# Kernel tuning notes

Measured on AMD Instinct MI355X. Metric: run time of the kernel, lower is better.

Reference implementation:

```python
import jax, jax.numpy as jnp
import numpy as np

N, F, H, D, E, G = 100000, 128, 2, 32, 1600000, 2048
HD = H * D
NEG_SLOPE = 0.2


def setup_inputs() -> dict:
    key = jax.random.key(0)
    ks = jax.random.split(key, 9)
    node = jax.random.normal(ks[0], (N, F), jnp.float32)
    edge_index = jax.random.randint(ks[1], (2, E), 0, N, dtype=jnp.int32)
    batch = jnp.sort(jax.random.randint(ks[2], (N,), 0, G, dtype=jnp.int32))
    # GATConv params
    W_gat = jax.random.normal(ks[3], (F, HD), jnp.float32) * (1.0 / np.sqrt(F))
    att_src = jax.random.normal(ks[4], (H, D), jnp.float32) * (1.0 / np.sqrt(D))
    att_dst = jax.random.normal(ks[5], (H, D), jnp.float32) * (1.0 / np.sqrt(D))
    bias_gat = jnp.zeros((HD,), jnp.float32)
    # SAGPooling score GNN = GraphConv(HD -> 1)
    W_rel = jax.random.normal(ks[6], (HD, 1), jnp.float32) * (1.0 / np.sqrt(HD))
    b_rel = jnp.zeros((1,), jnp.float32)
    W_root = jax.random.normal(ks[7], (HD, 1), jnp.float32) * (1.0 / np.sqrt(HD))
    return dict(node=node, edge_index=edge_index, batch=batch, W_gat=W_gat,
                att_src=att_src, att_dst=att_dst, bias_gat=bias_gat,
                W_rel=W_rel, b_rel=b_rel, W_root=W_root)


def _segment_softmax(logits, seg, num_segments):
    m = jax.ops.segment_max(logits, seg, num_segments=num_segments)
    e = jnp.exp(logits - m[seg])
    s = jax.ops.segment_sum(e, seg, num_segments=num_segments)
    return e / s[seg]


def reference(node, edge_index, batch, W_gat, att_src, att_dst, bias_gat,
              W_rel, b_rel, W_root):
    # ---- GATConv (heads=H, concat) with self-loops (PyG default) ----
    loops = jnp.arange(N, dtype=edge_index.dtype)
    src = jnp.concatenate([edge_index[0], loops])   # [E+N]
    dst = jnp.concatenate([edge_index[1], loops])   # [E+N]
    xw = (node @ W_gat).reshape(N, H, D)            # [N,H,D]
    a_src = jnp.einsum('nhd,hd->nh', xw, att_src)   # [N,H]
    a_dst = jnp.einsum('nhd,hd->nh', xw, att_dst)   # [N,H]
    logits = jax.nn.leaky_relu(a_src[src] + a_dst[dst], NEG_SLOPE)  # [E+N,H]
    alpha = _segment_softmax(logits, dst, N)        # softmax over incoming edges
    msg = xw[src] * alpha[:, :, None]               # [E+N,H,D]
    x = jax.ops.segment_sum(msg, dst, num_segments=N).reshape(N, HD) + bias_gat

    # ---- SAGPooling(min_score=-1): GraphConv score, per-graph softmax ----
    # GraphConv: out_i = W_root x_i + W_rel * sum_{j->i} x_j + b
    agg = jax.ops.segment_sum(x[edge_index[0]], edge_index[1], num_segments=N)
    score = (agg @ W_rel + b_rel + x @ W_root).reshape(-1)  # [N]
    score = _segment_softmax(score, batch, G)
    # min_score=-1 and softmax(score) >= 0 => all nodes survive top-k filter
    att_x = x * score[:, None]

    # ---- global_add_pool ----
    global_graph_emb = jax.ops.segment_sum(att_x, batch, num_segments=G)  # [G,HD]
    return (x, global_graph_emb)
```

## Files before the change

### kernel.cpp

```cpp
#include <hip/hip_runtime.h>
#include <hip/hip_fp16.h>

#define N_NODES 100000
#define F_IN    128
#define HDIM    64
#define NE      1600000
#define NG      2048
#define NEG_SLOPE 0.2f
#define DCAP    48
#define NB      3125
#define BCAP    768
#define NS2     512
#define SE2     (NE / NS2)
#define SCB     64
#define SCT     128

typedef unsigned short ushort_t;
typedef short bf16x8 __attribute__((ext_vector_type(8)));
typedef float f32x4 __attribute__((ext_vector_type(4)));

__device__ __forceinline__ ushort_t f2bf(float x) {
    unsigned u = __float_as_uint(x);
    unsigned r = u + 0x7fffu + ((u >> 16) & 1u);
    return (ushort_t)(r >> 16);
}
__device__ __forceinline__ float bf2f(ushort_t b) {
    return __uint_as_float(((unsigned)b) << 16);
}
__device__ __forceinline__ float f16lo(unsigned u) {
    __half hh = *(__half*)&u;
    return __half2float(hh);
}


__global__ __launch_bounds__(256) void k_hist(const int* __restrict__ ei,
        int* __restrict__ hist, const float* __restrict__ Wg,
        ushort_t* __restrict__ Wpack, const int* __restrict__ batch,
        int* __restrict__ gstart) {
    __shared__ int hc[NB];
    int t = threadIdx.x, b = blockIdx.x;
    if (b < NS2) {
        for (int i = t; i < NB; i += 256) hc[i] = 0;
        __syncthreads();
        int e0 = b * SE2;
        for (int e = e0 + t; e < e0 + SE2; e += 256)
            atomicAdd(&hc[ei[NE + e] >> 5], 1);
        __syncthreads();
        for (int i = t; i < NB; i += 256) hist[b * NB + i] = hc[i];
    } else if (b < NS2 + 32) {
        int i = (b - NS2) * 256 + t;
        int frag = i >> 9, lane = (i >> 3) & 63, j = i & 7;
        int ct = frag >> 2, kt = frag & 3;
        int k = kt * 32 + (lane >> 4) * 8 + j;
        int c = ct * 16 + (lane & 15);
        Wpack[i] = f2bf(Wg[k * HDIM + c]);
    } else {
        int n = (b - NS2 - 32) * 256 + t;
        if (n < N_NODES) {
            int bn = batch[n];
            int bp = (n == 0) ? -1 : batch[n - 1];
            for (int g = bp + 1; g <= bn; ++g) gstart[g] = n;
            if (n == N_NODES - 1)
                for (int g = bn + 1; g <= NG; ++g) gstart[g] = N_NODES;
        }
    }
}

__global__ __launch_bounds__(256) void k_scan(int* __restrict__ hist,
        int* __restrict__ bcnt) {
    __shared__ int tile[SCT][SCB + 1];
    int t = threadIdx.x;
    int b0 = blockIdx.x * SCB;
    int col = t & 63;
    int gb = b0 + col;
    bool own = (t < 64) && (gb < NB);
    int carry = own ? gb * BCAP : 0;

    for (int tile0 = 0; tile0 < NS2; tile0 += SCT) {
        for (int r = 0; r < SCT; r += 4) {
            int s = r + (t >> 6);
            int bb = b0 + col;
            tile[s][col] = (bb < NB) ? hist[(tile0 + s) * NB + bb] : 0;
        }
        __syncthreads();
        if (t < 64) {
            int c = carry;
#pragma unroll 8
            for (int s = 0; s < SCT; ++s) {
                int v = tile[s][col];
                tile[s][col] = c;
                c += v;
            }
            carry = c;
        }
        __syncthreads();
        for (int r = 0; r < SCT; r += 4) {
            int s = r + (t >> 6);
            int bb = b0 + col;
            if (bb < NB) hist[(tile0 + s) * NB + bb] = tile[s][col];
        }
        __syncthreads();
    }
    if (own) bcnt[gb] = carry - gb * BCAP;
}

__global__ __launch_bounds__(256) void k_scatter(const int* __restrict__ ei,
        const int* __restrict__ off, int* __restrict__ ebuf) {
    __shared__ int cursor[NB];
    int t = threadIdx.x;
    int bid = blockIdx.x;
    int b = ((bid & 7) << 6) | (bid >> 3);
    for (int i = t; i < NB; i += 256) cursor[i] = off[b * NB + i];
    __syncthreads();
    int e0 = b * SE2;
    for (int e = e0 + t; e < e0 + SE2; e += 256) {
        int d = ei[NE + e];
        int s = ei[e];
        int bb = d >> 5;
        int pos = atomicAdd(&cursor[bb], 1);
        if (pos < (bb + 1) * BCAP) ebuf[pos] = s | ((d & 31) << 17);
    }
}

__global__ __launch_bounds__(256) void k_gemm(const float* __restrict__ node,
        const ushort_t* __restrict__ Wpack, const float* __restrict__ att_s,
        const float* __restrict__ att_d, ushort_t* __restrict__ xw,
        float* __restrict__ a_src, float* __restrict__ a_dst) {
    int t = threadIdx.x;
    int lane = t & 63, w = t >> 6;
    int r0 = blockIdx.x * 64 + w * 16;

    int arow = r0 + (lane & 15);
    int arow_c = arow < N_NODES ? arow : N_NODES - 1;
    const float* nr = node + (size_t)arow_c * F_IN + (lane >> 4) * 8;

    bf16x8 a[4];
#pragma unroll
    for (int kt = 0; kt < 4; ++kt) {
        float4 v0 = *(const float4*)(nr + kt * 32);
        float4 v1 = *(const float4*)(nr + kt * 32 + 4);
        bf16x8 av;
        av[0] = (short)f2bf(v0.x); av[1] = (short)f2bf(v0.y);
        av[2] = (short)f2bf(v0.z); av[3] = (short)f2bf(v0.w);
        av[4] = (short)f2bf(v1.x); av[5] = (short)f2bf(v1.y);
        av[6] = (short)f2bf(v1.z); av[7] = (short)f2bf(v1.w);
        a[kt] = av;
    }

    const bf16x8* wp = (const bf16x8*)Wpack;
    float sv[2][4], dv[2][4];
#pragma unroll
    for (int h = 0; h < 2; ++h)
#pragma unroll
        for (int jj = 0; jj < 4; ++jj) { sv[h][jj] = 0.f; dv[h][jj] = 0.f; }

#pragma unroll
    for (int ct = 0; ct < 4; ++ct) {
        f32x4 acc = {0.f, 0.f, 0.f, 0.f};
#pragma unroll
        for (int kt = 0; kt < 4; ++kt) {
            bf16x8 bfr = wp[(ct * 4 + kt) * 64 + lane];
            acc = __builtin_amdgcn_mfma_f32_16x16x32_bf16(a[kt], bfr, acc, 0, 0, 0);
        }
        int col = ct * 16 + (lane & 15);
        float as_c = att_s[col];
        float ad_c = att_d[col];
        int h = ct >> 1;
#pragma unroll
        for (int jj = 0; jj < 4; ++jj) {
            int r = r0 + (lane >> 4) * 4 + jj;
            if (r < N_NODES) xw[(size_t)r * HDIM + col] = f2bf(acc[jj]);
            sv[h][jj] += acc[jj] * as_c;
            dv[h][jj] += acc[jj] * ad_c;
        }
    }

#pragma unroll
    for (int m = 1; m <= 8; m <<= 1) {
#pragma unroll
        for (int h = 0; h < 2; ++h)
#pragma unroll
            for (int jj = 0; jj < 4; ++jj) {
                sv[h][jj] += __shfl_xor(sv[h][jj], m, 64);
                dv[h][jj] += __shfl_xor(dv[h][jj], m, 64);
            }
    }
    if ((lane & 15) == 0) {
        int g = lane >> 4;
#pragma unroll
        for (int jj = 0; jj < 4; ++jj) {
            int r = r0 + g * 4 + jj;
            if (r < N_NODES) {
                a_src[r * 2 + 0] = sv[0][jj];
                a_src[r * 2 + 1] = sv[1][jj];
                a_dst[r * 2 + 0] = dv[0][jj];
                a_dst[r * 2 + 1] = dv[1][jj];
            }
        }
    }
}

__global__ __launch_bounds__(256) void k_gat(const int* __restrict__ bcnt,
        const int* __restrict__ ebuf, const ushort_t* __restrict__ xw,
        const float* __restrict__ a_src, const float* __restrict__ a_dst,
        const float* __restrict__ bias, const float* __restrict__ wrel,
        const float* __restrict__ wroot, const float* __restrict__ brel,
        float* __restrict__ x_out, float* __restrict__ p,
        float* __restrict__ base) {
    __shared__ int2 rows[32][DCAP];
    __shared__ int rowcnt[32];
    __shared__ float adld[64];
    int t = threadIdx.x, b = blockIdx.x;
    if (t < 32) rowcnt[t] = 0;
    if (t < 64) adld[t] = a_dst[b * 64 + t];
    __syncthreads();

    int cnt = bcnt[b]; if (cnt > BCAP) cnt = BCAP;
    const int* eb = ebuf + b * BCAP;
    for (int i = t; i < cnt; i += 256) {
        int v = eb[i];
        int s = v & 0x1FFFF;
        int dl = v >> 17;
        float2 asp = *(const float2*)(a_src + 2 * s);
        float l0 = asp.x + adld[2 * dl];     l0 = l0 > 0.f ? l0 : NEG_SLOPE * l0;
        float l1 = asp.y + adld[2 * dl + 1]; l1 = l1 > 0.f ? l1 : NEG_SLOPE * l1;
        __half2 hp = __floats2half2_rn(__expf(l0), __expf(l1));
        int pos = atomicAdd(&rowcnt[dl], 1);
        if (pos < DCAP) rows[dl][pos] = make_int2(s, *(int*)&hp);
    }
    __syncthreads();

    int lane = t & 63, wv = t >> 6;
    int h = lane >> 5;
    unsigned shift = (lane & 32) >> 1;
    const ushort_t* xwl = xw + lane;
    float bias_l = bias[lane];
    float wrel_l = wrel[lane];
    float wroot_l = wroot[lane];
    float br = brel[0];

#pragma unroll
    for (int q8 = 0; q8 < 8; ++q8) {
        int dl = wv * 8 + q8;
        int d = b * 32 + dl;
        int nv = rowcnt[dl]; if (nv > DCAP) nv = DCAP;
        const int2* rw = rows[dl];
        float acc = 0.f, den = 0.f;
        int j = 0;
        for (; j + 4 <= nv; j += 4) {
            int2 q0 = rw[j], q1 = rw[j + 1], q2 = rw[j + 2], q3 = rw[j + 3];
            ushort_t x0 = xwl[(size_t)q0.x * HDIM];
            ushort_t x1 = xwl[(size_t)q1.x * HDIM];
            ushort_t x2 = xwl[(size_t)q2.x * HDIM];
            ushort_t x3 = xwl[(size_t)q3.x * HDIM];
            float w0 = f16lo(((unsigned)q0.y) >> shift);
            float w1 = f16lo(((unsigned)q1.y) >> shift);
            float w2 = f16lo(((unsigned)q2.y) >> shift);
            float w3 = f16lo(((unsigned)q3.y) >> shift);
            acc += w0 * bf2f(x0); den += w0;
            acc += w1 * bf2f(x1); den += w1;
            acc += w2 * bf2f(x2); den += w2;
            acc += w3 * bf2f(x3); den += w3;
        }
        for (; j < nv; ++j) {
            int2 q0 = rw[j];
            float w0 = f16lo(((unsigned)q0.y) >> shift);
            acc += w0 * bf2f(xwl[(size_t)q0.x * HDIM]); den += w0;
        }

        float2 asd = *(const float2*)(a_src + 2 * d);
        float lgs = (h ? asd.y : asd.x) + adld[2 * dl + h];
        lgs = lgs > 0.f ? lgs : NEG_SLOPE * lgs;
        float es = __expf(lgs);
        float xself = bf2f(xw[(size_t)d * HDIM + lane]);
        float v = (acc + es * xself) / (den + es) + bias_l;
        x_out[(size_t)d * HDIM + lane] = v;

        float pv = v * wrel_l;
        float rv = v * wroot_l;
#pragma unroll
        for (int m = 32; m >= 1; m >>= 1) {
            pv += __shfl_xor(pv, m, 64);
            rv += __shfl_xor(rv, m, 64);
        }
        if (lane == 0) { p[d] = pv; base[d] = rv + br; }
    }
}

__global__ __launch_bounds__(256) void k_score(const int* __restrict__ bcnt,
        const int* __restrict__ ebuf, const float* __restrict__ pp,
        const float* __restrict__ base, float* __restrict__ evec) {
    __shared__ float sa[32];
    int t = threadIdx.x, b = blockIdx.x;
    if (t < 32) sa[t] = 0.f;
    __syncthreads();
    int cnt = bcnt[b]; if (cnt > BCAP) cnt = BCAP;
    const int* eb = ebuf + b * BCAP;
    for (int i = t; i < cnt; i += 256) {
        int v = eb[i];
        atomicAdd(&sa[v >> 17], pp[v & 0x1FFFF]);
    }
    __syncthreads();
    if (t < 32) {
        int n = b * 32 + t;
        evec[n] = __expf(sa[t] + base[n]);
    }
}

__global__ __launch_bounds__(256) void k_pool(const float* __restrict__ x,
        const float* __restrict__ evec, const int* __restrict__ gstart,
        float* __restrict__ emb) {
    int g = blockIdx.x;
    int lane = threadIdx.x & 63;
    int wave = threadIdx.x >> 6;
    int beg = gstart[g], end = gstart[g + 1];
    float acc = 0.f, esum = 0.f;
    for (int n = beg + wave; n < end; n += 4) {
        float ev = evec[n];
        acc += ev * x[(size_t)n * HDIM + lane];
        esum += ev;
    }
    __shared__ float sacc[4][HDIM];
    __shared__ float ses[4];
    sacc[wave][lane] = acc;
    if (lane == 0) ses[wave] = esum;
    __syncthreads();
    if (wave == 0) {
        float a = sacc[0][lane] + sacc[1][lane] + sacc[2][lane] + sacc[3][lane];
        float es = ses[0] + ses[1] + ses[2] + ses[3];
        emb[(size_t)g * HDIM + lane] = (es > 0.f) ? (a / es) : 0.f;
    }
}

extern "C" void kernel_launch(void* const* d_in, const int* in_sizes, int n_in,
                              void* d_out, int out_size, void* d_ws, size_t ws_size,
                              hipStream_t stream) {
    const float* node  = (const float*)d_in[0];
    const int*   ei    = (const int*)d_in[1];
    const int*   batch = (const int*)d_in[2];
    const float* Wg    = (const float*)d_in[3];
    const float* att_s = (const float*)d_in[4];
    const float* att_d = (const float*)d_in[5];
    const float* bias  = (const float*)d_in[6];
    const float* wrel  = (const float*)d_in[7];
    const float* brel  = (const float*)d_in[8];
    const float* wroot = (const float*)d_in[9];

    float* out = (float*)d_out;
    float* emb = out + (size_t)N_NODES * HDIM;

    float*    ws     = (float*)d_ws;
    ushort_t* Wpack  = (ushort_t*)ws;
    ushort_t* xw     = (ushort_t*)(ws + 4096);
    float*    a_src  = ws + 3204096;
    float*    a_dst  = ws + 3404096;
    float*    p      = ws + 3604096;
    float*    base   = ws + 3704096;
    float*    evec   = ws + 3804096;
    int*      gstart = (int*)(ws + 3904096);
    int*      bcnt   = (int*)(ws + 3906148);
    int*      ebuf   = (int*)(ws + 3909280);
    int*      hist   = (int*)(ws + 6309280);

    k_hist<<<NS2 + 32 + 391, 256, 0, stream>>>(ei, hist, Wg, Wpack, batch, gstart);
    k_scan<<<(NB + SCB - 1) / SCB, 256, 0, stream>>>(hist, bcnt);
    k_scatter<<<NS2, 256, 0, stream>>>(ei, hist, ebuf);
    k_gemm<<<(N_NODES + 63) / 64, 256, 0, stream>>>(node, Wpack, att_s, att_d,
                                                    xw, a_src, a_dst);
    k_gat<<<NB, 256, 0, stream>>>(bcnt, ebuf, xw, a_src, a_dst,
                                  bias, wrel, wroot, brel, out, p, base);
    k_score<<<NB, 256, 0, stream>>>(bcnt, ebuf, p, base, evec);
    k_pool<<<NG, 256, 0, stream>>>(out, evec, gstart, emb);
}
```

Before: 157.9 us.

## Fuse GEMM into front kernel and gather two bf16 columns per lane in GAT

```diff
diff --git a/kernel.cpp b/kernel.cpp
--- a/kernel.cpp
+++ b/kernel.cpp
@@ -14,6 +14,7 @@
 #define SE2     (NE / NS2)
 #define SCB     64
 #define SCT     128
+#define GEMM_BLKS 1563
 
 typedef unsigned short ushort_t;
 typedef short bf16x8 __attribute__((ext_vector_type(8)));
@@ -33,29 +34,107 @@
 }
 
 
-__global__ __launch_bounds__(256) void k_hist(const int* __restrict__ ei,
-        int* __restrict__ hist, const float* __restrict__ Wg,
-        ushort_t* __restrict__ Wpack, const int* __restrict__ batch,
-        int* __restrict__ gstart) {
-    __shared__ int hc[NB];
+__global__ __launch_bounds__(256) void k_front(const float* __restrict__ node,
+        const float* __restrict__ Wg, const float* __restrict__ att_s,
+        const float* __restrict__ att_d, ushort_t* __restrict__ xw,
+        float* __restrict__ a_src, float* __restrict__ a_dst,
+        const int* __restrict__ ei, int* __restrict__ hist,
+        const int* __restrict__ batch, int* __restrict__ gstart) {
+    __shared__ __align__(16) char smem[16384];
     int t = threadIdx.x, b = blockIdx.x;
-    if (b < NS2) {
+    if (b < GEMM_BLKS) {
+        ushort_t* WL = (ushort_t*)smem;
+        for (int i = t; i < 8192; i += 256) {
+            int frag = i >> 9, ln = (i >> 3) & 63, j = i & 7;
+            int ct = frag >> 2, kt = frag & 3;
+            int k = kt * 32 + (ln >> 4) * 8 + j;
+            int c = ct * 16 + (ln & 15);
+            WL[i] = f2bf(Wg[k * HDIM + c]);
+        }
+        __syncthreads();
+
+        int lane = t & 63, w = t >> 6;
+        int r0 = b * 64 + w * 16;
+        int arow = r0 + (lane & 15);
+        int arow_c = arow < N_NODES ? arow : N_NODES - 1;
+        const float* nr = node + (size_t)arow_c * F_IN + (lane >> 4) * 8;
+
+        bf16x8 a[4];
+#pragma unroll
+        for (int kt = 0; kt < 4; ++kt) {
+            float4 v0 = *(const float4*)(nr + kt * 32);
+            float4 v1 = *(const float4*)(nr + kt * 32 + 4);
+            bf16x8 av;
+            av[0] = (short)f2bf(v0.x); av[1] = (short)f2bf(v0.y);
+            av[2] = (short)f2bf(v0.z); av[3] = (short)f2bf(v0.w);
+            av[4] = (short)f2bf(v1.x); av[5] = (short)f2bf(v1.y);
+            av[6] = (short)f2bf(v1.z); av[7] = (short)f2bf(v1.w);
+            a[kt] = av;
+        }
+
+        const bf16x8* wp = (const bf16x8*)WL;
+        float sv[2][4], dv[2][4];
+#pragma unroll
+        for (int h = 0; h < 2; ++h)
+#pragma unroll
+            for (int jj = 0; jj < 4; ++jj) { sv[h][jj] = 0.f; dv[h][jj] = 0.f; }
+
+#pragma unroll
+        for (int ct = 0; ct < 4; ++ct) {
+            f32x4 acc = {0.f, 0.f, 0.f, 0.f};
+#pragma unroll
+            for (int kt = 0; kt < 4; ++kt) {
+                bf16x8 bfr = wp[(ct * 4 + kt) * 64 + lane];
+                acc = __builtin_amdgcn_mfma_f32_16x16x32_bf16(a[kt], bfr, acc, 0, 0, 0);
+            }
+            int col = ct * 16 + (lane & 15);
+            float as_c = att_s[col];
+            float ad_c = att_d[col];
+            int h = ct >> 1;
+#pragma unroll
+            for (int jj = 0; jj < 4; ++jj) {
+                int r = r0 + (lane >> 4) * 4 + jj;
+                if (r < N_NODES) xw[(size_t)r * HDIM + col] = f2bf(acc[jj]);
+                sv[h][jj] += acc[jj] * as_c;
+                dv[h][jj] += acc[jj] * ad_c;
+            }
+        }
+
+#pragma unroll
+        for (int m = 1; m <= 8; m <<= 1) {
+#pragma unroll
+            for (int h = 0; h < 2; ++h)
+#pragma unroll
+                for (int jj = 0; jj < 4; ++jj) {
+                    sv[h][jj] += __shfl_xor(sv[h][jj], m, 64);
+                    dv[h][jj] += __shfl_xor(dv[h][jj], m, 64);
+                }
+        }
+        if ((lane & 15) == 0) {
+            int g = lane >> 4;
+#pragma unroll
+            for (int jj = 0; jj < 4; ++jj) {
+                int r = r0 + g * 4 + jj;
+                if (r < N_NODES) {
+                    a_src[r * 2 + 0] = sv[0][jj];
+                    a_src[r * 2 + 1] = sv[1][jj];
+                    a_dst[r * 2 + 0] = dv[0][jj];
+                    a_dst[r * 2 + 1] = dv[1][jj];
+                }
+            }
+        }
+    } else if (b < GEMM_BLKS + NS2) {
+        int* hc = (int*)smem;
+        int bb = b - GEMM_BLKS;
         for (int i = t; i < NB; i += 256) hc[i] = 0;
         __syncthreads();
-        int e0 = b * SE2;
+        int e0 = bb * SE2;
         for (int e = e0 + t; e < e0 + SE2; e += 256)
             atomicAdd(&hc[ei[NE + e] >> 5], 1);
         __syncthreads();
-        for (int i = t; i < NB; i += 256) hist[b * NB + i] = hc[i];
-    } else if (b < NS2 + 32) {
-        int i = (b - NS2) * 256 + t;
-        int frag = i >> 9, lane = (i >> 3) & 63, j = i & 7;
-        int ct = frag >> 2, kt = frag & 3;
-        int k = kt * 32 + (lane >> 4) * 8 + j;
-        int c = ct * 16 + (lane & 15);
-        Wpack[i] = f2bf(Wg[k * HDIM + c]);
+        for (int i = t; i < NB; i += 256) hist[bb * NB + i] = hc[i];
     } else {
-        int n = (b - NS2 - 32) * 256 + t;
+        int n = (b - GEMM_BLKS - NS2) * 256 + t;
         if (n < N_NODES) {
             int bn = batch[n];
             int bp = (n == 0) ? -1 : batch[n - 1];
@@ -119,84 +198,6 @@
         int bb = d >> 5;
         int pos = atomicAdd(&cursor[bb], 1);
         if (pos < (bb + 1) * BCAP) ebuf[pos] = s | ((d & 31) << 17);
-    }
-}
-
-__global__ __launch_bounds__(256) void k_gemm(const float* __restrict__ node,
-        const ushort_t* __restrict__ Wpack, const float* __restrict__ att_s,
-        const float* __restrict__ att_d, ushort_t* __restrict__ xw,
-        float* __restrict__ a_src, float* __restrict__ a_dst) {
-    int t = threadIdx.x;
-    int lane = t & 63, w = t >> 6;
-    int r0 = blockIdx.x * 64 + w * 16;
-
-    int arow = r0 + (lane & 15);
-    int arow_c = arow < N_NODES ? arow : N_NODES - 1;
-    const float* nr = node + (size_t)arow_c * F_IN + (lane >> 4) * 8;
-
-    bf16x8 a[4];
-#pragma unroll
-    for (int kt = 0; kt < 4; ++kt) {
-        float4 v0 = *(const float4*)(nr + kt * 32);
-        float4 v1 = *(const float4*)(nr + kt * 32 + 4);
-        bf16x8 av;
-        av[0] = (short)f2bf(v0.x); av[1] = (short)f2bf(v0.y);
-        av[2] = (short)f2bf(v0.z); av[3] = (short)f2bf(v0.w);
-        av[4] = (short)f2bf(v1.x); av[5] = (short)f2bf(v1.y);
-        av[6] = (short)f2bf(v1.z); av[7] = (short)f2bf(v1.w);
-        a[kt] = av;
-    }
-
-    const bf16x8* wp = (const bf16x8*)Wpack;
-    float sv[2][4], dv[2][4];
-#pragma unroll
-    for (int h = 0; h < 2; ++h)
-#pragma unroll
-        for (int jj = 0; jj < 4; ++jj) { sv[h][jj] = 0.f; dv[h][jj] = 0.f; }
-
-#pragma unroll
-    for (int ct = 0; ct < 4; ++ct) {
-        f32x4 acc = {0.f, 0.f, 0.f, 0.f};
-#pragma unroll
-        for (int kt = 0; kt < 4; ++kt) {
-            bf16x8 bfr = wp[(ct * 4 + kt) * 64 + lane];
-            acc = __builtin_amdgcn_mfma_f32_16x16x32_bf16(a[kt], bfr, acc, 0, 0, 0);
-        }
-        int col = ct * 16 + (lane & 15);
-        float as_c = att_s[col];
-        float ad_c = att_d[col];
-        int h = ct >> 1;
-#pragma unroll
-        for (int jj = 0; jj < 4; ++jj) {
-            int r = r0 + (lane >> 4) * 4 + jj;
-            if (r < N_NODES) xw[(size_t)r * HDIM + col] = f2bf(acc[jj]);
-            sv[h][jj] += acc[jj] * as_c;
-            dv[h][jj] += acc[jj] * ad_c;
-        }
-    }
-
-#pragma unroll
-    for (int m = 1; m <= 8; m <<= 1) {
-#pragma unroll
-        for (int h = 0; h < 2; ++h)
-#pragma unroll
-            for (int jj = 0; jj < 4; ++jj) {
-                sv[h][jj] += __shfl_xor(sv[h][jj], m, 64);
-                dv[h][jj] += __shfl_xor(dv[h][jj], m, 64);
-            }
-    }
-    if ((lane & 15) == 0) {
-        int g = lane >> 4;
-#pragma unroll
-        for (int jj = 0; jj < 4; ++jj) {
-            int r = r0 + g * 4 + jj;
-            if (r < N_NODES) {
-                a_src[r * 2 + 0] = sv[0][jj];
-                a_src[r * 2 + 1] = sv[1][jj];
-                a_dst[r * 2 + 0] = dv[0][jj];
-                a_dst[r * 2 + 1] = dv[1][jj];
-            }
-        }
     }
 }
 
@@ -226,17 +227,20 @@
         float l1 = asp.y + adld[2 * dl + 1]; l1 = l1 > 0.f ? l1 : NEG_SLOPE * l1;
         __half2 hp = __floats2half2_rn(__expf(l0), __expf(l1));
         int pos = atomicAdd(&rowcnt[dl], 1);
-        if (pos < DCAP) rows[dl][pos] = make_int2(s, *(int*)&hp);
+        if (pos < DCAP) rows[dl][pos] = make_int2(s << 7, *(int*)&hp);
     }
     __syncthreads();
 
     int lane = t & 63, wv = t >> 6;
-    int h = lane >> 5;
-    unsigned shift = (lane & 32) >> 1;
-    const ushort_t* xwl = xw + lane;
-    float bias_l = bias[lane];
-    float wrel_l = wrel[lane];
-    float wroot_l = wroot[lane];
+    int half = lane >> 5;
+    int li = lane & 31;
+    int h2 = li >> 4;
+    unsigned shift = (unsigned)(li & 16);
+    unsigned colOff = (unsigned)(li << 2);
+    const char* xwB = (const char*)xw;
+    float2 bias2  = *(const float2*)(bias + 2 * li);
+    float2 wrel2  = *(const float2*)(wrel + 2 * li);
+    float2 wroot2 = *(const float2*)(wroot + 2 * li);
     float br = brel[0];
 
 #pragma unroll
@@ -245,39 +249,52 @@
         int d = b * 32 + dl;
         int nv = rowcnt[dl]; if (nv > DCAP) nv = DCAP;
         const int2* rw = rows[dl];
-        float acc = 0.f, den = 0.f;
+        float aL0 = 0.f, aH0 = 0.f, aL1 = 0.f, aH1 = 0.f, den = 0.f;
         int j = 0;
         for (; j + 4 <= nv; j += 4) {
-            int2 q0 = rw[j], q1 = rw[j + 1], q2 = rw[j + 2], q3 = rw[j + 3];
-            ushort_t x0 = xwl[(size_t)q0.x * HDIM];
-            ushort_t x1 = xwl[(size_t)q1.x * HDIM];
-            ushort_t x2 = xwl[(size_t)q2.x * HDIM];
-            ushort_t x3 = xwl[(size_t)q3.x * HDIM];
-            float w0 = f16lo(((unsigned)q0.y) >> shift);
-            float w1 = f16lo(((unsigned)q1.y) >> shift);
-            float w2 = f16lo(((unsigned)q2.y) >> shift);
-            float w3 = f16lo(((unsigned)q3.y) >> shift);
-            acc += w0 * bf2f(x0); den += w0;
-            acc += w1 * bf2f(x1); den += w1;
-            acc += w2 * bf2f(x2); den += w2;
-            acc += w3 * bf2f(x3); den += w3;
-        }
-        for (; j < nv; ++j) {
-            int2 q0 = rw[j];
-            float w0 = f16lo(((unsigned)q0.y) >> shift);
-            acc += w0 * bf2f(xwl[(size_t)q0.x * HDIM]); den += w0;
-        }
+            int2 qa = rw[j + half];
+            int2 qb = rw[j + 2 + half];
+            unsigned ua = *(const unsigned*)(xwB + ((unsigned)qa.x + colOff));
+            unsigned ub = *(const unsigned*)(xwB + ((unsigned)qb.x + colOff));
+            float wa = f16lo(((unsigned)qa.y) >> shift);
+            float wb = f16lo(((unsigned)qb.y) >> shift);
+            aL0 += wa * __uint_as_float(ua << 16);
+            aH0 += wa * __uint_as_float(ua & 0xFFFF0000u);
+            den += wa;
+            aL1 += wb * __uint_as_float(ub << 16);
+            aH1 += wb * __uint_as_float(ub & 0xFFFF0000u);
+            den += wb;
+        }
+        for (; j < nv; j += 2) {
+            int jj = j + half;
+            if (jj < nv) {
+                int2 qa = rw[jj];
+                unsigned ua = *(const unsigned*)(xwB + ((unsigned)qa.x + colOff));
+                float wa = f16lo(((unsigned)qa.y) >> shift);
+                aL0 += wa * __uint_as_float(ua << 16);
+                aH0 += wa * __uint_as_float(ua & 0xFFFF0000u);
+                den += wa;
+            }
+        }
+        float accL = aL0 + aL1, accH = aH0 + aH1;
+        accL += __shfl_xor(accL, 32, 64);
+        accH += __shfl_xor(accH, 32, 64);
+        den  += __shfl_xor(den, 32, 64);
 
         float2 asd = *(const float2*)(a_src + 2 * d);
-        float lgs = (h ? asd.y : asd.x) + adld[2 * dl + h];
+        float lgs = (h2 ? asd.y : asd.x) + adld[2 * dl + h2];
         lgs = lgs > 0.f ? lgs : NEG_SLOPE * lgs;
         float es = __expf(lgs);
-        float xself = bf2f(xw[(size_t)d * HDIM + lane]);
-        float v = (acc + es * xself) / (den + es) + bias_l;
-        x_out[(size_t)d * HDIM + lane] = v;
-
-        float pv = v * wrel_l;
-        float rv = v * wroot_l;
+        unsigned us = *(const unsigned*)(xwB + (((unsigned)d << 7) + colOff));
+        float denT = den + es;
+        float vL = (accL + es * __uint_as_float(us << 16)) / denT + bias2.x;
+        float vH = (accH + es * __uint_as_float(us & 0xFFFF0000u)) / denT + bias2.y;
+        if (half == 0)
+            *(float2*)(x_out + (size_t)d * HDIM + 2 * li) = make_float2(vL, vH);
+
+        float pv = vL * wrel2.x + vH * wrel2.y;
+        float rv = vL * wroot2.x + vH * wroot2.y;
+        if (half) { pv = 0.f; rv = 0.f; }
 #pragma unroll
         for (int m = 32; m >= 1; m >>= 1) {
             pv += __shfl_xor(pv, m, 64);
@@ -350,7 +367,6 @@
     float* emb = out + (size_t)N_NODES * HDIM;
 
     float*    ws     = (float*)d_ws;
-    ushort_t* Wpack  = (ushort_t*)ws;
     ushort_t* xw     = (ushort_t*)(ws + 4096);
     float*    a_src  = ws + 3204096;
     float*    a_dst  = ws + 3404096;
@@ -362,11 +378,11 @@
     int*      ebuf   = (int*)(ws + 3909280);
     int*      hist   = (int*)(ws + 6309280);
 
-    k_hist<<<NS2 + 32 + 391, 256, 0, stream>>>(ei, hist, Wg, Wpack, batch, gstart);
+    k_front<<<GEMM_BLKS + NS2 + 391, 256, 0, stream>>>(node, Wg, att_s, att_d,
+                                                       xw, a_src, a_dst,
+                                                       ei, hist, batch, gstart);
     k_scan<<<(NB + SCB - 1) / SCB, 256, 0, stream>>>(hist, bcnt);
     k_scatter<<<NS2, 256, 0, stream>>>(ei, hist, ebuf);
-    k_gemm<<<(N_NODES + 63) / 64, 256, 0, stream>>>(node, Wpack, att_s, att_d,
-                                                    xw, a_src, a_dst);
     k_gat<<<NB, 256, 0, stream>>>(bcnt, ebuf, xw, a_src, a_dst,
                                   bias, wrel, wroot, brel, out, p, base);
     k_score<<<NB, 256, 0, stream>>>(bcnt, ebuf, p, base, evec);
```

Measured after the change: 155.4 us. Within noise of the previous version (-1.6%).
